# Optimization experiments

Hardware: AMD Instinct MI355X
Metric: run time of the kernel (lower is better)

## Reference

```python
import jax, jax.numpy as jnp
import numpy as np

B, N, C, T = 8, 207, 2, 12
E, HEADS, L, FF = 64, 4, 2, 4
TOUT = 12
N_GAT_HEADS = 8
ALPHA = 0.2
NEG = -9e15


def layer_norm(x, g, b, eps=1e-5):
    mu = x.mean(-1, keepdims=True)
    var = x.var(-1, keepdims=True)
    return (x - mu) / jnp.sqrt(var + eps) * g + b


def setup_inputs() -> dict:
    key = jax.random.key(0)
    ks = iter(jax.random.split(key, 40))

    def rn(shape, s=0.1):
        return jax.random.normal(next(ks), shape, jnp.float32) * s

    return {
        "x": jax.random.normal(next(ks), (B, C, N, T), jnp.float32),
        "adj": jax.random.randint(next(ks), (B, N, N), 0, 2, jnp.int32),
        # GraphAttention params per head (W1 is dead code in the original: omitted)
        "gat_W2": rn((N_GAT_HEADS, 2 * C, C), 0.5),
        "gat_a": rn((N_GAT_HEADS, C), 0.5),
        "gat_b": rn((N_GAT_HEADS, C), 0.1),
        "conv1_w": rn((2 * C, E), 0.3),   # 1x1 conv: [in, out]
        "conv1_b": rn((E,), 0.1),
        "temb": rn((288, E), 0.1),        # temporal embedding table [time_num, E]
        "Wq": rn((L, E, E), 0.12), "Wk": rn((L, E, E), 0.12), "Wv": rn((L, E, E), 0.12),
        "Wo": rn((L, E, E), 0.12), "bo": rn((L, E), 0.02),
        "ln1_g": jnp.ones((L, E)), "ln1_b": jnp.zeros((L, E)),
        "ln2_g": jnp.ones((L, E)), "ln2_b": jnp.zeros((L, E)),
        "ff_w1": rn((L, E, FF * E), 0.12), "ff_b1": rn((L, FF * E), 0.02),
        "ff_w2": rn((L, FF * E, E), 0.12), "ff_b2": rn((L, E), 0.02),
        "lng": jnp.ones((L, E)), "lnb": jnp.zeros((L, E)),
        "conv2_w": rn((TOUT, T), 0.2), "conv2_b": rn((TOUT,), 0.05),
        "conv3_w": rn((E,), 0.2), "conv3_b": rn((1,), 0.05),
    }


def reference(x, adj, gat_W2, gat_a, gat_b, conv1_w, conv1_b, temb,
              Wq, Wk, Wv, Wo, bo, ln1_g, ln1_b, ln2_g, ln2_b,
              ff_w1, ff_b1, ff_w2, ff_b2, lng, lnb,
              conv2_w, conv2_b, conv3_w, conv3_b):
    # ---- GAT applied independently per time step; fold T into batch ----
    xb = x.transpose(0, 3, 2, 1).reshape(B * T, N, C)      # [BT,N,C]
    adjb = jnp.repeat(adj, T, axis=0)                       # [BT,N,N]
    # Faithful replication of repeat_interleave / repeat + cat(dim=1) + view
    # (note: the original concatenates along dim=1 then views, which scrambles
    #  the pairwise layout; jnp reshape reproduces the identical memory view)
    comb = jnp.concatenate([jnp.repeat(xb, N, axis=1),
                            jnp.tile(xb, (1, N, 1))], axis=1).reshape(B * T, N, N, 2 * C)
    acc = jnp.zeros((B * T, N, C), x.dtype)
    for h in range(N_GAT_HEADS):  # heads have distinct params; fixed small loop
        wx = jnp.einsum('bijc,ce->bije', comb, gat_W2[h])           # [BT,N,N,C]
        e = jnp.einsum('bije,e->bij', jax.nn.leaky_relu(wx, ALPHA), gat_a[h])
        att = jax.nn.softmax(jnp.where(adjb > 0, e, NEG), axis=-1)  # [BT,N,N]
        acc = acc + jnp.tanh(jnp.einsum('bij,bjc->bic', att, xb) + gat_b[h])
    gat_out = (acc / N_GAT_HEADS).reshape(B, T, N, C)       # average aggregate

    # ---- conv1 on cat([x, GAT_feature], channel) ----
    gat_feat = gat_out.transpose(0, 3, 2, 1)                # [B,C,N,T]
    xcat = jnp.concatenate([x, gat_feat], axis=1)           # [B,2C,N,T]
    out = jnp.einsum('bcnt,ce->bnte', xcat, conv1_w) + conv1_b  # [B,N,T,E]

    # ---- temporal transformer encoder ----
    dk = E // HEADS
    scale = np.float32(1.0 / np.sqrt(dk))
    d_t = temb[:T]                                          # [T,E]
    for l in range(L):
        qq = out + d_t
        Q = (qq @ Wq[l]).reshape(B, N, T, HEADS, dk).transpose(0, 3, 1, 2, 4)
        K = (qq @ Wk[l]).reshape(B, N, T, HEADS, dk).transpose(0, 3, 1, 2, 4)
        V = (qq @ Wv[l]).reshape(B, N, T, HEADS, dk).transpose(0, 3, 1, 2, 4)
        att = jax.nn.softmax(jnp.einsum('bhntd,bhnsd->bhnts', Q, K) * scale, axis=-1)
        ctx = jnp.einsum('bhnts,bhnsd->bhntd', att, V)
        ctx = ctx.transpose(0, 2, 3, 1, 4).reshape(B, N, T, E)
        attn_out = ctx @ Wo[l] + bo[l]
        x1 = layer_norm(attn_out + qq, ln1_g[l], ln1_b[l])
        ff = jax.nn.relu(x1 @ ff_w1[l] + ff_b1[l]) @ ff_w2[l] + ff_b2[l]
        blk = layer_norm(ff + x1, ln2_g[l], ln2_b[l])
        out = layer_norm(blk + out, lng[l], lnb[l])         # outer layer norm1 residual

    # ---- output convs ----
    ot = out.transpose(0, 2, 1, 3)                          # [B,T,N,E]
    o2 = jax.nn.relu(jnp.einsum('btne,ot->bone', ot, conv2_w)
                     + conv2_b[None, :, None, None])        # [B,TOUT,N,E]
    final = jnp.einsum('btne,e->bnt', o2, conv3_w) + conv3_b[0]  # [B,N,TOUT]
    return final
```

## Files before the change

kernel.cpp:

```cpp
#include <hip/hip_runtime.h>
#include <hip/hip_bf16.h>

#define NN   207
#define BB   8
#define TT   12
#define EE   64
#define FFD  256
#define NGH  8
#define GALPHA 0.2f
#define GNEG  -9e15f

#define SRD   68
#define SRD16 72
#define FSRD  264
#define L_QQ  0
#define L_X1  816
#define L_QB  1632
#define L_KB  2064
#define L_VB  2496
#define L_SC  2928
#define L_CTX 3504
#define L_FF  1632
#define L_TOTB 4800

__device__ __forceinline__ float lo_f(unsigned u) { return __uint_as_float(u << 16); }
__device__ __forceinline__ float hi_f(unsigned u) { return __uint_as_float(u & 0xffff0000u); }
__device__ __forceinline__ float b16f(unsigned short s) { return __uint_as_float(((unsigned)s) << 16); }
__device__ __forceinline__ unsigned pk2(float a, float b) {
  unsigned la = (unsigned)__bfloat16_as_ushort(__float2bfloat16(a));
  unsigned lb = (unsigned)__bfloat16_as_ushort(__float2bfloat16(b));
  return la | (lb << 16);
}
__device__ __forceinline__ unsigned short bf16u(float a) {
  return __bfloat16_as_ushort(__float2bfloat16(a));
}
__device__ __forceinline__ float tanh_fast(float x) {
  return 1.f - 2.f * __builtin_amdgcn_rcpf(__expf(2.f * x) + 1.f);
}

__device__ __forceinline__ float row16_sum(float v) {
  v += __int_as_float(__builtin_amdgcn_update_dpp(0, __float_as_int(v), 0x121, 0xf, 0xf, false));
  v += __int_as_float(__builtin_amdgcn_update_dpp(0, __float_as_int(v), 0x122, 0xf, 0xf, false));
  v += __int_as_float(__builtin_amdgcn_update_dpp(0, __float_as_int(v), 0x124, 0xf, 0xf, false));
  v += __int_as_float(__builtin_amdgcn_update_dpp(0, __float_as_int(v), 0x128, 0xf, 0xf, false));
  return v;
}
__device__ __forceinline__ float wave_sum(float v) {
  const float r = row16_sum(v);
  const float a = __int_as_float(__builtin_amdgcn_readlane(__float_as_int(r), 0));
  const float b = __int_as_float(__builtin_amdgcn_readlane(__float_as_int(r), 16));
  const float c = __int_as_float(__builtin_amdgcn_readlane(__float_as_int(r), 32));
  const float d = __int_as_float(__builtin_amdgcn_readlane(__float_as_int(r), 48));
  return (a + b) + (c + d);
}
#define UNPK8(U, f) { (f)[0]=lo_f((U).x); (f)[1]=hi_f((U).x); (f)[2]=lo_f((U).y); (f)[3]=hi_f((U).y); \
                      (f)[4]=lo_f((U).z); (f)[5]=hi_f((U).z); (f)[6]=lo_f((U).w); (f)[7]=hi_f((U).w); }


__global__ __launch_bounds__(256) void prep_weights(
    const float* __restrict__ Wq, const float* __restrict__ Wk,
    const float* __restrict__ Wv, const float* __restrict__ Wo,
    const float* __restrict__ ff_w1, const float* __restrict__ ff_w2,
    unsigned short* __restrict__ wb)
{
  const int idx = blockIdx.x * 256 + threadIdx.x;
  float v;
  if (idx < 32768) {
    const int which = idx >> 13;
    const int r = idx & 8191;
    const int l = r >> 12, q = r & 4095;
    const int kb = q >> 9, c = (q >> 3) & 63, j = q & 7;
    const float* W = (which == 0) ? Wq : (which == 1) ? Wk : (which == 2) ? Wv : Wo;
    v = W[l*4096 + (8*kb + j)*64 + c];
  } else if (idx < 65536) {
    const int r = idx - 32768;
    const int l = r >> 14, q = r & 16383;
    const int kb = q >> 11, f = (q >> 3) & 255, j = q & 7;
    v = ff_w1[l*16384 + (8*kb + j)*256 + f];
  } else {
    const int r = idx - 65536;
    const int l = r >> 14, q = r & 16383;
    const int kb = q >> 9, e = (q >> 3) & 63, j = q & 7;
    v = ff_w2[l*16384 + (8*kb + j)*64 + e];
  }
  wb[idx] = bf16u(v);
}

#define A_GW 2484

__global__ __launch_bounds__(256) void gat_conv1_kernel(
    const float* __restrict__ x,        const int* __restrict__ adj,
    const float* __restrict__ gat_W2,   const float* __restrict__ gat_a,
    const float* __restrict__ gat_b,    const float* __restrict__ conv1_w,
    const float* __restrict__ conv1_b,  unsigned short* __restrict__ out0)
{
  __shared__ float lds[A_GW + 96];
  unsigned* au = (unsigned*)lds;

  const int bn   = blockIdx.x;
  const int b    = bn / NN;
  const int i    = bn % NN;
  const int tid  = threadIdx.x;
  const int lane = tid & 63;
  const int wid  = tid >> 6;

  const float* xb = x + b * 2 * NN * TT;
  for (int idx = tid; idx < NN * TT; idx += 256) {
    const int n = idx / TT, t = idx % TT;
    au[t * NN + n] = pk2(xb[idx], xb[NN * TT + idx]);
  }
  if (tid < 64) lds[A_GW + tid] = gat_W2[tid];
  if (tid < 16) { lds[A_GW + 64 + tid] = gat_a[tid]; lds[A_GW + 80 + tid] = gat_b[tid]; }
  __syncthreads();

  float aokf[4];
  int   row0[4], row1[4];
  {
    const int NSQ = NN * NN;
#pragma unroll
    for (int q = 0; q < 4; ++q) {
      const int j = lane + 64 * q;
      const int jj = (j < NN) ? j : 0;
      const int r0 = 2 * (i * NN + jj), r1 = r0 + 1;
      row0[q] = (r0 < NSQ) ? (r0 / NN) : ((r0 - NSQ) % NN);
      row1[q] = (r1 < NSQ) ? (r1 / NN) : ((r1 - NSQ) % NN);
      aokf[q] = ((j < NN) && adj[(b * NN + i) * NN + jj] > 0) ? 1.f : 0.f;
    }
  }

  float xr00[3][4], xr01[3][4], xr10[3][4], xr11[3][4], xj0[3][4], xj1[3][4];
#pragma unroll
  for (int tk = 0; tk < 3; ++tk) {
    const unsigned* xst = au + (wid + 4 * tk) * NN;
#pragma unroll
    for (int q = 0; q < 4; ++q) {
      int j = lane + 64 * q; if (j >= NN) j = 0;
      const unsigned u0 = xst[row0[q]], u1 = xst[row1[q]], uj = xst[j];
      xr00[tk][q] = lo_f(u0); xr01[tk][q] = hi_f(u0);
      xr10[tk][q] = lo_f(u1); xr11[tk][q] = hi_f(u1);
      xj0[tk][q]  = lo_f(uj); xj1[tk][q]  = hi_f(uj);
    }
  }

  float acc0[3] = {0.f, 0.f, 0.f}, acc1[3] = {0.f, 0.f, 0.f};
#pragma unroll 1
  for (int h = 0; h < NGH; ++h) {
    const float w0 = lds[A_GW + h*8 + 0], w1_ = lds[A_GW + h*8 + 1];
    const float w2_= lds[A_GW + h*8 + 2], w3  = lds[A_GW + h*8 + 3];
    const float w4 = lds[A_GW + h*8 + 4], w5  = lds[A_GW + h*8 + 5];
    const float w6 = lds[A_GW + h*8 + 6], w7  = lds[A_GW + h*8 + 7];
    const float a0 = lds[A_GW + 64 + h*2], a1 = lds[A_GW + 64 + h*2 + 1];
    const float gb0 = lds[A_GW + 80 + h*2], gb1 = lds[A_GW + 80 + h*2 + 1];
    float s0[3] = {0.f,0.f,0.f}, s1[3] = {0.f,0.f,0.f}, s2[3] = {0.f,0.f,0.f};
#pragma unroll
    for (int tk = 0; tk < 3; ++tk) {
#pragma unroll
      for (int q = 0; q < 4; ++q) {
        float wx0 = xr00[tk][q]*w0 + xr01[tk][q]*w2_ + xr10[tk][q]*w4 + xr11[tk][q]*w6;
        float wx1 = xr00[tk][q]*w1_ + xr01[tk][q]*w3 + xr10[tk][q]*w5 + xr11[tk][q]*w7;
        wx0 = (wx0 > 0.f) ? wx0 : GALPHA * wx0;
        wx1 = (wx1 > 0.f) ? wx1 : GALPHA * wx1;
        float e = a0 * wx0 + a1 * wx1;
        e = (aokf[q] > 0.f) ? e : GNEG;
        const float ex = __expf(e);
        s0[tk] += ex; s1[tk] += ex * xj0[tk][q]; s2[tk] += ex * xj1[tk][q];
      }
    }
#pragma unroll
    for (int tk = 0; tk < 3; ++tk) {
      const float d0 = wave_sum(s0[tk]);
      const float d1 = wave_sum(s1[tk]);
      const float d2 = wave_sum(s2[tk]);
      const float inv = __builtin_amdgcn_rcpf(d0);
      acc0[tk] += tanh_fast(d1 * inv + gb0);
      acc1[tk] += tanh_fast(d2 * inv + gb1);
    }
  }

  {
    const float c1w0 = conv1_w[lane],       c1w1 = conv1_w[64 + lane];
    const float c1w2 = conv1_w[128 + lane], c1w3 = conv1_w[192 + lane];
    const float c1b  = conv1_b[lane];
#pragma unroll
    for (int tk = 0; tk < 3; ++tk) {
      const int t = wid + 4 * tk;
      const unsigned up = au[t * NN + i];
      const float g0 = acc0[tk] * (1.f / NGH), g1 = acc1[tk] * (1.f / NGH);
      out0[bn*768 + t*EE + lane] =
          bf16u(lo_f(up)*c1w0 + hi_f(up)*c1w1 + g0*c1w2 + g1*c1w3 + c1b);
    }
  }
}

__global__ __launch_bounds__(256) void xf_final_kernel(
    const unsigned short* __restrict__ out0,
    const unsigned short* __restrict__ wb,
    const float* __restrict__ temb,
    const float* __restrict__ bo,
    const float* __restrict__ ln1_g, const float* __restrict__ ln1_b,
    const float* __restrict__ ln2_g, const float* __restrict__ ln2_b,
    const float* __restrict__ ff_b1, const float* __restrict__ ff_b2,
    const float* __restrict__ lng, const float* __restrict__ lnb,
    const float* __restrict__ conv2_w, const float* __restrict__ conv2_b,
    const float* __restrict__ conv3_w, const float* __restrict__ conv3_b,
    float* __restrict__ fout)
{
  __shared__ float lds[L_TOTB];
  unsigned*       au   = (unsigned*)lds;
  unsigned short* sh16 = (unsigned short*)lds;

  const int bn   = blockIdx.x;
  const int tid  = threadIdx.x;
  const int lane = tid & 63;
  const int wid  = tid >> 6;
  const int t0   = 3 * wid;

  float outv[3];
#pragma unroll
  for (int tt = 0; tt < 3; ++tt)
    outv[tt] = b16f(out0[bn*768 + (t0 + tt)*EE + lane]);

  for (int l = 0; l < 2; ++l) {
    const unsigned short* wqt = wb + l*4096;
    const unsigned short* wkt = wb + 8192  + l*4096;
    const unsigned short* wvt = wb + 16384 + l*4096;
    const unsigned short* wot = wb + 24576 + l*4096;
    const unsigned short* w1t = wb + 32768 + l*16384;
    const unsigned short* w2t = wb + 65536 + l*16384;

    __syncthreads();

    float qqv[3];
#pragma unroll
    for (int tt = 0; tt < 3; ++tt) {
      qqv[tt] = outv[tt] + temb[(t0 + tt)*EE + lane];
      lds[L_QQ + (t0 + tt)*SRD + lane] = qqv[tt];
    }

    {
      const int c = lane;
      float aq[3] = {0,0,0}, ak[3] = {0,0,0}, av[3] = {0,0,0};
      const unsigned short* wqp = wqt + c*8;
      const unsigned short* wkp = wkt + c*8;
      const unsigned short* wvp = wvt + c*8;
#pragma unroll 1
      for (int kb = 0; kb < 8; ++kb) {
        const uint4 wq4 = *(const uint4*)(wqp + kb*512);
        const uint4 wk4 = *(const uint4*)(wkp + kb*512);
        const uint4 wv4 = *(const uint4*)(wvp + kb*512);
        float a[3][8];
#pragma unroll
        for (int tt = 0; tt < 3; ++tt) {
          *(float4*)&a[tt][0] = *(const float4*)&lds[L_QQ + (t0+tt)*SRD + 8*kb];
          *(float4*)&a[tt][4] = *(const float4*)&lds[L_QQ + (t0+tt)*SRD + 8*kb + 4];
        }
        float wf[8];
        UNPK8(wq4, wf);
#pragma unroll
        for (int tt = 0; tt < 3; ++tt)
#pragma unroll
          for (int j = 0; j < 8; ++j) aq[tt] += a[tt][j]*wf[j];
        UNPK8(wk4, wf);
#pragma unroll
        for (int tt = 0; tt < 3; ++tt)
#pragma unroll
          for (int j = 0; j < 8; ++j) ak[tt] += a[tt][j]*wf[j];
        UNPK8(wv4, wf);
#pragma unroll
        for (int tt = 0; tt < 3; ++tt)
#pragma unroll
          for (int j = 0; j < 8; ++j) av[tt] += a[tt][j]*wf[j];
      }
#pragma unroll
      for (int tt = 0; tt < 3; ++tt) {
        const int t = t0 + tt;
        sh16[2*L_QB + t*SRD16 + c] = bf16u(aq[tt]);
        sh16[2*L_KB + t*SRD16 + c] = bf16u(ak[tt]);
        sh16[2*L_VB + t*SRD16 + c] = bf16u(av[tt]);
      }
    }
    __syncthreads();

    {
      const int h = wid;
      if (lane < 48) {
        const int t = lane >> 2, s0 = 3*(lane & 3);
        float qf[16];
        {
          const uint4 qa = *(const uint4*)&sh16[2*L_QB + t*SRD16 + h*16];
          const uint4 qb = *(const uint4*)&sh16[2*L_QB + t*SRD16 + h*16 + 8];
          UNPK8(qa, qf); UNPK8(qb, qf + 8);
        }
#pragma unroll
        for (int ss = 0; ss < 3; ++ss) {
          const int s = s0 + ss;
          float d = 0.f;
          {
            const uint4 ka = *(const uint4*)&sh16[2*L_KB + s*SRD16 + h*16];
            float kf[8]; UNPK8(ka, kf);
#pragma unroll
            for (int xq = 0; xq < 8; ++xq) d += qf[xq]*kf[xq];
          }
          {
            const uint4 kc = *(const uint4*)&sh16[2*L_KB + s*SRD16 + h*16 + 8];
            float kf[8]; UNPK8(kc, kf);
#pragma unroll
            for (int xq = 0; xq < 8; ++xq) d += qf[8+xq]*kf[xq];
          }
          lds[L_SC + h*144 + t*12 + s] = d * 0.25f;
        }
      }
      __builtin_amdgcn_wave_barrier();
      if (lane < 12) {
        float* row = &lds[L_SC + h*144 + lane*12];
        float m = row[0];
#pragma unroll
        for (int s = 1; s < 12; ++s) m = fmaxf(m, row[s]);
        float ex[12]; float sum = 0.f;
#pragma unroll
        for (int s = 0; s < 12; ++s) { ex[s] = __expf(row[s] - m); sum += ex[s]; }
        const float inv = __builtin_amdgcn_rcpf(sum);
#pragma unroll
        for (int s = 0; s < 12; ++s) row[s] = ex[s] * inv;
      }
      __builtin_amdgcn_wave_barrier();
      {
        const int d = lane & 15, tq = lane >> 4;
#pragma unroll
        for (int tt = 0; tt < 3; ++tt) {
          const int t = tq + 4*tt;
          float cacc = 0.f;
#pragma unroll
          for (int s = 0; s < 12; ++s) {
            const float p = lds[L_SC + h*144 + t*12 + s];
            const unsigned uv = au[L_VB + s*36 + h*8 + (d >> 1)];
            cacc += p * ((d & 1) ? hi_f(uv) : lo_f(uv));
          }
          lds[L_CTX + t*SRD + h*16 + d] = cacc;
        }
      }
    }
    __syncthreads();

    {
      float acc[3] = {0,0,0};
      const unsigned short* wop = wot + lane*8;
#pragma unroll 1
      for (int kb = 0; kb < 8; ++kb) {
        const uint4 w4 = *(const uint4*)(wop + kb*512);
        float a[3][8];
#pragma unroll
        for (int tt = 0; tt < 3; ++tt) {
          *(float4*)&a[tt][0] = *(const float4*)&lds[L_CTX + (t0+tt)*SRD + 8*kb];
          *(float4*)&a[tt][4] = *(const float4*)&lds[L_CTX + (t0+tt)*SRD + 8*kb + 4];
        }
        float wf[8]; UNPK8(w4, wf);
#pragma unroll
        for (int tt = 0; tt < 3; ++tt)
#pragma unroll
          for (int j = 0; j < 8; ++j) acc[tt] += a[tt][j]*wf[j];
      }
#pragma unroll
      for (int tt = 0; tt < 3; ++tt) {
        float v = acc[tt] + bo[l*EE + lane] + qqv[tt];
        const float mu = wave_sum(v) * (1.f/64);
        const float dd = v - mu;
        const float var = wave_sum(dd*dd) * (1.f/64);
        lds[L_X1 + (t0+tt)*SRD + lane] =
            dd * rsqrtf(var + 1e-5f) * ln1_g[l*EE + lane] + ln1_b[l*EE + lane];
      }
    }
    __syncthreads();

    {
      const int f0 = 4*lane;
      float ac[4][3] = {};
#pragma unroll 1
      for (int kb = 0; kb < 8; ++kb) {
        uint4 w4[4];
#pragma unroll
        for (int ff = 0; ff < 4; ++ff)
          w4[ff] = *(const uint4*)(w1t + kb*2048 + (f0+ff)*8);
        float a[3][8];
#pragma unroll
        for (int tt = 0; tt < 3; ++tt) {
          *(float4*)&a[tt][0] = *(const float4*)&lds[L_X1 + (t0+tt)*SRD + 8*kb];
          *(float4*)&a[tt][4] = *(const float4*)&lds[L_X1 + (t0+tt)*SRD + 8*kb + 4];
        }
#pragma unroll
        for (int ff = 0; ff < 4; ++ff) {
          float wf[8]; UNPK8(w4[ff], wf);
#pragma unroll
          for (int tt = 0; tt < 3; ++tt)
#pragma unroll
            for (int j = 0; j < 8; ++j) ac[ff][tt] += a[tt][j]*wf[j];
        }
      }
      const float4 bv = *(const float4*)&ff_b1[l*FFD + f0];
#pragma unroll
      for (int tt = 0; tt < 3; ++tt) {
        *(float4*)&lds[L_FF + (t0+tt)*FSRD + f0] = make_float4(
            fmaxf(ac[0][tt] + bv.x, 0.f), fmaxf(ac[1][tt] + bv.y, 0.f),
            fmaxf(ac[2][tt] + bv.z, 0.f), fmaxf(ac[3][tt] + bv.w, 0.f));
      }
    }

    {
      float acc[3] = {0,0,0};
      const unsigned short* w2p = w2t + lane*8;
#pragma unroll 1
      for (int kb = 0; kb < 32; ++kb) {
        const uint4 w4 = *(const uint4*)(w2p + kb*512);
        float a[3][8];
#pragma unroll
        for (int tt = 0; tt < 3; ++tt) {
          *(float4*)&a[tt][0] = *(const float4*)&lds[L_FF + (t0+tt)*FSRD + 8*kb];
          *(float4*)&a[tt][4] = *(const float4*)&lds[L_FF + (t0+tt)*FSRD + 8*kb + 4];
        }
        float wf[8]; UNPK8(w4, wf);
#pragma unroll
        for (int tt = 0; tt < 3; ++tt)
#pragma unroll
          for (int j = 0; j < 8; ++j) acc[tt] += a[tt][j]*wf[j];
      }
#pragma unroll
      for (int tt = 0; tt < 3; ++tt) {
        float v = acc[tt] + ff_b2[l*EE + lane] + lds[L_X1 + (t0+tt)*SRD + lane];
        float mu = wave_sum(v) * (1.f/64);
        float dd = v - mu;
        float var = wave_sum(dd*dd) * (1.f/64);
        const float blk = dd * rsqrtf(var + 1e-5f) * ln2_g[l*EE + lane] + ln2_b[l*EE + lane];
        float w = blk + outv[tt];
        mu = wave_sum(w) * (1.f/64);
        dd = w - mu;
        var = wave_sum(dd*dd) * (1.f/64);
        outv[tt] = dd * rsqrtf(var + 1e-5f) * lng[l*EE + lane] + lnb[l*EE + lane];
      }
    }
  }

#pragma unroll
  for (int tt = 0; tt < 3; ++tt)
    lds[L_QQ + (t0+tt)*SRD + lane] = outv[tt];
  __syncthreads();

  float xt[12];
#pragma unroll
  for (int t = 0; t < 12; ++t) xt[t] = lds[L_QQ + t*SRD + lane];
  const float c3w = conv3_w[lane];
  for (int o = wid; o < 12; o += 4) {
    float a = conv2_b[o];
#pragma unroll
    for (int t = 0; t < 12; ++t) a += xt[t] * conv2_w[o*TT + t];
    a = fmaxf(a, 0.f);
    const float s = wave_sum(a * c3w);
    if (lane == 0) fout[bn*TT + o] = s + conv3_b[0];
  }
}

extern "C" void kernel_launch(void* const* d_in, const int* in_sizes, int n_in,
                              void* d_out, int out_size, void* d_ws, size_t ws_size,
                              hipStream_t stream) {
  const float* x       = (const float*)d_in[0];
  const int*   adj     = (const int*)  d_in[1];
  const float* gat_W2  = (const float*)d_in[2];
  const float* gat_a   = (const float*)d_in[3];
  const float* gat_b   = (const float*)d_in[4];
  const float* conv1_w = (const float*)d_in[5];
  const float* conv1_b = (const float*)d_in[6];
  const float* temb    = (const float*)d_in[7];
  const float* Wq      = (const float*)d_in[8];
  const float* Wk      = (const float*)d_in[9];
  const float* Wv      = (const float*)d_in[10];
  const float* Wo      = (const float*)d_in[11];
  const float* bo      = (const float*)d_in[12];
  const float* ln1_g   = (const float*)d_in[13];
  const float* ln1_b   = (const float*)d_in[14];
  const float* ln2_g   = (const float*)d_in[15];
  const float* ln2_b   = (const float*)d_in[16];
  const float* ff_w1   = (const float*)d_in[17];
  const float* ff_b1   = (const float*)d_in[18];
  const float* ff_w2   = (const float*)d_in[19];
  const float* ff_b2   = (const float*)d_in[20];
  const float* lng     = (const float*)d_in[21];
  const float* lnb     = (const float*)d_in[22];
  const float* conv2_w = (const float*)d_in[23];
  const float* conv2_b = (const float*)d_in[24];
  const float* conv3_w = (const float*)d_in[25];
  const float* conv3_b = (const float*)d_in[26];

  unsigned short* wb   = (unsigned short*)d_ws;
  unsigned short* out0 = wb + 98304;
  float* fout = (float*)d_out;

  prep_weights<<<384, 256, 0, stream>>>(Wq, Wk, Wv, Wo, ff_w1, ff_w2, wb);

  gat_conv1_kernel<<<BB*NN, 256, 0, stream>>>(
      x, adj, gat_W2, gat_a, gat_b, conv1_w, conv1_b, out0);

  xf_final_kernel<<<BB*NN, 256, 0, stream>>>(
      out0, wb, temb, bo, ln1_g, ln1_b, ln2_g, ln2_b,
      ff_b1, ff_b2, lng, lnb, conv2_w, conv2_b, conv3_w, conv3_b, fout);
}
```

Baseline: 283.9 us.

## Switch transformer matmuls to packed fp16 FMA with fp16 activations in LDS

Stores weights, the intermediate activation buffer and the LDS activations as fp16 instead of bf16/fp32, and runs the QKV, score, output projection and FFN dot products with packed half2 FMAs (v_pk_fma_f16) in place of unpacked fp32 FMAs. The LDS layout is redone with disjoint regions per tensor so some __syncthreads can be dropped, and the post-attention LN1 result is kept in registers. This roughly halves FMA instruction count and LDS traffic. The cost is fp16 accumulation, with a risk of lost precision or overflow over the 256-long FFN reductions.

```diff
diff --git a/kernel.cpp b/kernel.cpp
--- a/kernel.cpp
+++ b/kernel.cpp
@@ -1,5 +1,6 @@
 #include <hip/hip_runtime.h>
 #include <hip/hip_bf16.h>
+#include <hip/hip_fp16.h>
 
 #define NN   207
 #define BB   8
@@ -10,29 +11,29 @@
 #define GALPHA 0.2f
 #define GNEG  -9e15f
 
-#define SRD   68
-#define SRD16 72
-#define FSRD  264
-#define L_QQ  0
-#define L_X1  816
-#define L_QB  1632
-#define L_KB  2064
-#define L_VB  2496
-#define L_SC  2928
-#define L_CTX 3504
-#define L_FF  1632
-#define L_TOTB 4800
+#define U_QQ  0
+#define U_X1  864
+#define U_QB  1728
+#define U_KB  2592
+#define U_VB  3456
+#define F_SC  2160
+#define U_CTX 5472
+#define U_FF  6336
+#define F_FIN 3168
+#define LDS_F32 4752
 
 __device__ __forceinline__ float lo_f(unsigned u) { return __uint_as_float(u << 16); }
 __device__ __forceinline__ float hi_f(unsigned u) { return __uint_as_float(u & 0xffff0000u); }
-__device__ __forceinline__ float b16f(unsigned short s) { return __uint_as_float(((unsigned)s) << 16); }
 __device__ __forceinline__ unsigned pk2(float a, float b) {
   unsigned la = (unsigned)__bfloat16_as_ushort(__float2bfloat16(a));
   unsigned lb = (unsigned)__bfloat16_as_ushort(__float2bfloat16(b));
   return la | (lb << 16);
 }
-__device__ __forceinline__ unsigned short bf16u(float a) {
-  return __bfloat16_as_ushort(__float2bfloat16(a));
+__device__ __forceinline__ unsigned short h16u(float a) {
+  return __half_as_ushort(__float2half(a));
+}
+__device__ __forceinline__ float u16f(unsigned short s) {
+  return __half2float(__ushort_as_half(s));
 }
 __device__ __forceinline__ float tanh_fast(float x) {
   return 1.f - 2.f * __builtin_amdgcn_rcpf(__expf(2.f * x) + 1.f);
@@ -53,8 +54,6 @@
   const float d = __int_as_float(__builtin_amdgcn_readlane(__float_as_int(r), 48));
   return (a + b) + (c + d);
 }
-#define UNPK8(U, f) { (f)[0]=lo_f((U).x); (f)[1]=hi_f((U).x); (f)[2]=lo_f((U).y); (f)[3]=hi_f((U).y); \
-                      (f)[4]=lo_f((U).z); (f)[5]=hi_f((U).z); (f)[6]=lo_f((U).w); (f)[7]=hi_f((U).w); }
 
 
 __global__ __launch_bounds__(256) void prep_weights(
@@ -83,7 +82,7 @@
     const int kb = q >> 9, e = (q >> 3) & 63, j = q & 7;
     v = ff_w2[l*16384 + (8*kb + j)*64 + e];
   }
-  wb[idx] = bf16u(v);
+  wb[idx] = h16u(v);
 }
 
 #define A_GW 2484
@@ -187,7 +186,7 @@
       const unsigned up = au[t * NN + i];
       const float g0 = acc0[tk] * (1.f / NGH), g1 = acc1[tk] * (1.f / NGH);
       out0[bn*768 + t*EE + lane] =
-          bf16u(lo_f(up)*c1w0 + hi_f(up)*c1w1 + g0*c1w2 + g1*c1w3 + c1b);
+          h16u(lo_f(up)*c1w0 + hi_f(up)*c1w1 + g0*c1w2 + g1*c1w3 + c1b);
     }
   }
 }
@@ -205,7 +204,7 @@
     const float* __restrict__ conv3_w, const float* __restrict__ conv3_b,
     float* __restrict__ fout)
 {
-  __shared__ float lds[L_TOTB];
+  __shared__ float lds[LDS_F32];
   unsigned*       au   = (unsigned*)lds;
   unsigned short* sh16 = (unsigned short*)lds;
 
@@ -215,10 +214,12 @@
   const int wid  = tid >> 6;
   const int t0   = 3 * wid;
 
+  const __half2 hz = __floats2half2_rn(0.f, 0.f);
+
   float outv[3];
 #pragma unroll
   for (int tt = 0; tt < 3; ++tt)
-    outv[tt] = b16f(out0[bn*768 + (t0 + tt)*EE + lane]);
+    outv[tt] = u16f(out0[bn*768 + (t0 + tt)*EE + lane]);
 
   for (int l = 0; l < 2; ++l) {
     const unsigned short* wqt = wb + l*4096;
@@ -228,55 +229,49 @@
     const unsigned short* w1t = wb + 32768 + l*16384;
     const unsigned short* w2t = wb + 65536 + l*16384;
 
-    __syncthreads();
-
     float qqv[3];
 #pragma unroll
     for (int tt = 0; tt < 3; ++tt) {
       qqv[tt] = outv[tt] + temb[(t0 + tt)*EE + lane];
-      lds[L_QQ + (t0 + tt)*SRD + lane] = qqv[tt];
+      sh16[U_QQ + (t0 + tt)*72 + lane] = h16u(qqv[tt]);
     }
 
     {
-      const int c = lane;
-      float aq[3] = {0,0,0}, ak[3] = {0,0,0}, av[3] = {0,0,0};
-      const unsigned short* wqp = wqt + c*8;
-      const unsigned short* wkp = wkt + c*8;
-      const unsigned short* wvp = wvt + c*8;
+      const unsigned short* wqp = wqt + lane*8;
+      const unsigned short* wkp = wkt + lane*8;
+      const unsigned short* wvp = wvt + lane*8;
+      __half2 cq[3], ck[3], cv[3];
+#pragma unroll
+      for (int tt = 0; tt < 3; ++tt) { cq[tt] = hz; ck[tt] = hz; cv[tt] = hz; }
 #pragma unroll 1
       for (int kb = 0; kb < 8; ++kb) {
         const uint4 wq4 = *(const uint4*)(wqp + kb*512);
         const uint4 wk4 = *(const uint4*)(wkp + kb*512);
         const uint4 wv4 = *(const uint4*)(wvp + kb*512);
-        float a[3][8];
+        uint4 a4[3];
+#pragma unroll
+        for (int tt = 0; tt < 3; ++tt)
+          a4[tt] = *(const uint4*)&sh16[U_QQ + (t0+tt)*72 + 8*kb];
+        const __half2* wq2 = (const __half2*)&wq4;
+        const __half2* wk2 = (const __half2*)&wk4;
+        const __half2* wv2 = (const __half2*)&wv4;
 #pragma unroll
         for (int tt = 0; tt < 3; ++tt) {
-          *(float4*)&a[tt][0] = *(const float4*)&lds[L_QQ + (t0+tt)*SRD + 8*kb];
-          *(float4*)&a[tt][4] = *(const float4*)&lds[L_QQ + (t0+tt)*SRD + 8*kb + 4];
-        }
-        float wf[8];
-        UNPK8(wq4, wf);
-#pragma unroll
-        for (int tt = 0; tt < 3; ++tt)
-#pragma unroll
-          for (int j = 0; j < 8; ++j) aq[tt] += a[tt][j]*wf[j];
-        UNPK8(wk4, wf);
-#pragma unroll
-        for (int tt = 0; tt < 3; ++tt)
-#pragma unroll
-          for (int j = 0; j < 8; ++j) ak[tt] += a[tt][j]*wf[j];
-        UNPK8(wv4, wf);
-#pragma unroll
-        for (int tt = 0; tt < 3; ++tt)
-#pragma unroll
-          for (int j = 0; j < 8; ++j) av[tt] += a[tt][j]*wf[j];
+          const __half2* a2 = (const __half2*)&a4[tt];
+#pragma unroll
+          for (int j = 0; j < 4; ++j) {
+            cq[tt] = __hfma2(a2[j], wq2[j], cq[tt]);
+            ck[tt] = __hfma2(a2[j], wk2[j], ck[tt]);
+            cv[tt] = __hfma2(a2[j], wv2[j], cv[tt]);
+          }
+        }
       }
 #pragma unroll
       for (int tt = 0; tt < 3; ++tt) {
         const int t = t0 + tt;
-        sh16[2*L_QB + t*SRD16 + c] = bf16u(aq[tt]);
-        sh16[2*L_KB + t*SRD16 + c] = bf16u(ak[tt]);
-        sh16[2*L_VB + t*SRD16 + c] = bf16u(av[tt]);
+        sh16[U_QB + t*72 + lane] = h16u(__low2float(cq[tt]) + __high2float(cq[tt]));
+        sh16[U_KB + t*72 + lane] = h16u(__low2float(ck[tt]) + __high2float(ck[tt]));
+        sh16[U_VB + t*72 + lane] = h16u(__low2float(cv[tt]) + __high2float(cv[tt]));
       }
     }
     __syncthreads();
@@ -285,34 +280,29 @@
       const int h = wid;
       if (lane < 48) {
         const int t = lane >> 2, s0 = 3*(lane & 3);
-        float qf[16];
-        {
-          const uint4 qa = *(const uint4*)&sh16[2*L_QB + t*SRD16 + h*16];
-          const uint4 qb = *(const uint4*)&sh16[2*L_QB + t*SRD16 + h*16 + 8];
-          UNPK8(qa, qf); UNPK8(qb, qf + 8);
-        }
+        const uint4 qa = *(const uint4*)&sh16[U_QB + t*72 + h*16];
+        const uint4 qb = *(const uint4*)&sh16[U_QB + t*72 + h*16 + 8];
+        const __half2* q2a = (const __half2*)&qa;
+        const __half2* q2b = (const __half2*)&qb;
 #pragma unroll
         for (int ss = 0; ss < 3; ++ss) {
           const int s = s0 + ss;
-          float d = 0.f;
-          {
-            const uint4 ka = *(const uint4*)&sh16[2*L_KB + s*SRD16 + h*16];
-            float kf[8]; UNPK8(ka, kf);
-#pragma unroll
-            for (int xq = 0; xq < 8; ++xq) d += qf[xq]*kf[xq];
+          const uint4 ka = *(const uint4*)&sh16[U_KB + s*72 + h*16];
+          const uint4 kc = *(const uint4*)&sh16[U_KB + s*72 + h*16 + 8];
+          const __half2* k2a = (const __half2*)&ka;
+          const __half2* k2b = (const __half2*)&kc;
+          __half2 d2 = hz;
+#pragma unroll
+          for (int j = 0; j < 4; ++j) {
+            d2 = __hfma2(q2a[j], k2a[j], d2);
+            d2 = __hfma2(q2b[j], k2b[j], d2);
           }
-          {
-            const uint4 kc = *(const uint4*)&sh16[2*L_KB + s*SRD16 + h*16 + 8];
-            float kf[8]; UNPK8(kc, kf);
-#pragma unroll
-            for (int xq = 0; xq < 8; ++xq) d += qf[8+xq]*kf[xq];
-          }
-          lds[L_SC + h*144 + t*12 + s] = d * 0.25f;
+          lds[F_SC + h*144 + t*12 + s] = (__low2float(d2) + __high2float(d2)) * 0.25f;
         }
       }
       __builtin_amdgcn_wave_barrier();
       if (lane < 12) {
-        float* row = &lds[L_SC + h*144 + lane*12];
+        float* row = &lds[F_SC + h*144 + lane*12];
         float m = row[0];
 #pragma unroll
         for (int s = 1; s < 12; ++s) m = fmaxf(m, row[s]);
@@ -332,100 +322,130 @@
           float cacc = 0.f;
 #pragma unroll
           for (int s = 0; s < 12; ++s) {
-            const float p = lds[L_SC + h*144 + t*12 + s];
-            const unsigned uv = au[L_VB + s*36 + h*8 + (d >> 1)];
-            cacc += p * ((d & 1) ? hi_f(uv) : lo_f(uv));
+            const float p = lds[F_SC + h*144 + t*12 + s];
+            const unsigned uv = au[(U_VB/2) + s*36 + h*8 + (d >> 1)];
+            const __half2 hv = *(const __half2*)&uv;
+            cacc += p * ((d & 1) ? __high2float(hv) : __low2float(hv));
           }
-          lds[L_CTX + t*SRD + h*16 + d] = cacc;
+          sh16[U_CTX + t*72 + h*16 + d] = h16u(cacc);
         }
       }
     }
     __syncthreads();
 
+    float x1v[3];
     {
-      float acc[3] = {0,0,0};
       const unsigned short* wop = wot + lane*8;
+      __half2 co[3];
+#pragma unroll
+      for (int tt = 0; tt < 3; ++tt) co[tt] = hz;
 #pragma unroll 1
       for (int kb = 0; kb < 8; ++kb) {
         const uint4 w4 = *(const uint4*)(wop + kb*512);
-        float a[3][8];
+        const __half2* w2_ = (const __half2*)&w4;
+        uint4 a4[3];
+#pragma unroll
+        for (int tt = 0; tt < 3; ++tt)
+          a4[tt] = *(const uint4*)&sh16[U_CTX + (t0+tt)*72 + 8*kb];
 #pragma unroll
         for (int tt = 0; tt < 3; ++tt) {
-          *(float4*)&a[tt][0] = *(const float4*)&lds[L_CTX + (t0+tt)*SRD + 8*kb];
-          *(float4*)&a[tt][4] = *(const float4*)&lds[L_CTX + (t0+tt)*SRD + 8*kb + 4];
-        }
-        float wf[8]; UNPK8(w4, wf);
-#pragma unroll
-        for (int tt = 0; tt < 3; ++tt)
-#pragma unroll
-          for (int j = 0; j < 8; ++j) acc[tt] += a[tt][j]*wf[j];
+          const __half2* a2 = (const __half2*)&a4[tt];
+#pragma unroll
+          for (int j = 0; j < 4; ++j) co[tt] = __hfma2(a2[j], w2_[j], co[tt]);
+        }
       }
 #pragma unroll
       for (int tt = 0; tt < 3; ++tt) {
-        float v = acc[tt] + bo[l*EE + lane] + qqv[tt];
+        float v = __low2float(co[tt]) + __high2float(co[tt]) + bo[l*EE + lane] + qqv[tt];
         const float mu = wave_sum(v) * (1.f/64);
         const float dd = v - mu;
         const float var = wave_sum(dd*dd) * (1.f/64);
-        lds[L_X1 + (t0+tt)*SRD + lane] =
-            dd * rsqrtf(var + 1e-5f) * ln1_g[l*EE + lane] + ln1_b[l*EE + lane];
-      }
-    }
-    __syncthreads();
+        x1v[tt] = dd * rsqrtf(var + 1e-5f) * ln1_g[l*EE + lane] + ln1_b[l*EE + lane];
+        sh16[U_X1 + (t0+tt)*72 + lane] = h16u(x1v[tt]);
+      }
+    }
 
     {
       const int f0 = 4*lane;
-      float ac[4][3] = {};
+      __half2 c2[4][3];
+#pragma unroll
+      for (int ff = 0; ff < 4; ++ff)
+#pragma unroll
+        for (int tt = 0; tt < 3; ++tt) c2[ff][tt] = hz;
 #pragma unroll 1
       for (int kb = 0; kb < 8; ++kb) {
         uint4 w4[4];
 #pragma unroll
         for (int ff = 0; ff < 4; ++ff)
           w4[ff] = *(const uint4*)(w1t + kb*2048 + (f0+ff)*8);
-        float a[3][8];
-#pragma unroll
-        for (int tt = 0; tt < 3; ++tt) {
-          *(float4*)&a[tt][0] = *(const float4*)&lds[L_X1 + (t0+tt)*SRD + 8*kb];
-          *(float4*)&a[tt][4] = *(const float4*)&lds[L_X1 + (t0+tt)*SRD + 8*kb + 4];
-        }
+        uint4 a4[3];
+#pragma unroll
+        for (int tt = 0; tt < 3; ++tt)
+          a4[tt] = *(const uint4*)&sh16[U_X1 + (t0+tt)*72 + 8*kb];
 #pragma unroll
         for (int ff = 0; ff < 4; ++ff) {
-          float wf[8]; UNPK8(w4[ff], wf);
-#pragma unroll
-          for (int tt = 0; tt < 3; ++tt)
-#pragma unroll
-            for (int j = 0; j < 8; ++j) ac[ff][tt] += a[tt][j]*wf[j];
+          const __half2* w2_ = (const __half2*)&w4[ff];
+#pragma unroll
+          for (int tt = 0; tt < 3; ++tt) {
+            const __half2* a2 = (const __half2*)&a4[tt];
+#pragma unroll
+            for (int j = 0; j < 4; ++j) c2[ff][tt] = __hfma2(a2[j], w2_[j], c2[ff][tt]);
+          }
         }
       }
       const float4 bv = *(const float4*)&ff_b1[l*FFD + f0];
 #pragma unroll
       for (int tt = 0; tt < 3; ++tt) {
-        *(float4*)&lds[L_FF + (t0+tt)*FSRD + f0] = make_float4(
-            fmaxf(ac[0][tt] + bv.x, 0.f), fmaxf(ac[1][tt] + bv.y, 0.f),
-            fmaxf(ac[2][tt] + bv.z, 0.f), fmaxf(ac[3][tt] + bv.w, 0.f));
+        const float r0 = fmaxf(__low2float(c2[0][tt]) + __high2float(c2[0][tt]) + bv.x, 0.f);
+        const float r1 = fmaxf(__low2float(c2[1][tt]) + __high2float(c2[1][tt]) + bv.y, 0.f);
+        const float r2 = fmaxf(__low2float(c2[2][tt]) + __high2float(c2[2][tt]) + bv.z, 0.f);
+        const float r3 = fmaxf(__low2float(c2[3][tt]) + __high2float(c2[3][tt]) + bv.w, 0.f);
+        __half2 p01 = __floats2half2_rn(r0, r1);
+        __half2 p23 = __floats2half2_rn(r2, r3);
+        uint2 pk;
+        pk.x = *(unsigned*)&p01;
+        pk.y = *(unsigned*)&p23;
+        *(uint2*)&sh16[U_FF + (t0+tt)*264 + f0] = pk;
       }
     }
 
     {
-      float acc[3] = {0,0,0};
       const unsigned short* w2p = w2t + lane*8;
+      __half2 cA[3], cB[3];
+#pragma unroll
+      for (int tt = 0; tt < 3; ++tt) { cA[tt] = hz; cB[tt] = hz; }
 #pragma unroll 1
-      for (int kb = 0; kb < 32; ++kb) {
-        const uint4 w4 = *(const uint4*)(w2p + kb*512);
-        float a[3][8];
-#pragma unroll
-        for (int tt = 0; tt < 3; ++tt) {
-          *(float4*)&a[tt][0] = *(const float4*)&lds[L_FF + (t0+tt)*FSRD + 8*kb];
-          *(float4*)&a[tt][4] = *(const float4*)&lds[L_FF + (t0+tt)*FSRD + 8*kb + 4];
-        }
-        float wf[8]; UNPK8(w4, wf);
-#pragma unroll
-        for (int tt = 0; tt < 3; ++tt)
-#pragma unroll
-          for (int j = 0; j < 8; ++j) acc[tt] += a[tt][j]*wf[j];
+      for (int kp = 0; kp < 16; ++kp) {
+        {
+          const int kb = 2*kp;
+          const uint4 w4 = *(const uint4*)(w2p + kb*512);
+          const __half2* w2_ = (const __half2*)&w4;
+#pragma unroll
+          for (int tt = 0; tt < 3; ++tt) {
+            const uint4 a4 = *(const uint4*)&sh16[U_FF + (t0+tt)*264 + 8*kb];
+            const __half2* a2 = (const __half2*)&a4;
+#pragma unroll
+            for (int j = 0; j < 4; ++j) cA[tt] = __hfma2(a2[j], w2_[j], cA[tt]);
+          }
+        }
+        {
+          const int kb = 2*kp + 1;
+          const uint4 w4 = *(const uint4*)(w2p + kb*512);
+          const __half2* w2_ = (const __half2*)&w4;
+#pragma unroll
+          for (int tt = 0; tt < 3; ++tt) {
+            const uint4 a4 = *(const uint4*)&sh16[U_FF + (t0+tt)*264 + 8*kb];
+            const __half2* a2 = (const __half2*)&a4;
+#pragma unroll
+            for (int j = 0; j < 4; ++j) cB[tt] = __hfma2(a2[j], w2_[j], cB[tt]);
+          }
+        }
       }
 #pragma unroll
       for (int tt = 0; tt < 3; ++tt) {
-        float v = acc[tt] + ff_b2[l*EE + lane] + lds[L_X1 + (t0+tt)*SRD + lane];
+        float v = __low2float(cA[tt]) + __high2float(cA[tt])
+                + __low2float(cB[tt]) + __high2float(cB[tt])
+                + ff_b2[l*EE + lane] + x1v[tt];
         float mu = wave_sum(v) * (1.f/64);
         float dd = v - mu;
         float var = wave_sum(dd*dd) * (1.f/64);
@@ -439,14 +459,15 @@
     }
   }
 
+  __syncthreads();
 #pragma unroll
   for (int tt = 0; tt < 3; ++tt)
-    lds[L_QQ + (t0+tt)*SRD + lane] = outv[tt];
+    lds[F_FIN + (t0+tt)*68 + lane] = outv[tt];
   __syncthreads();
 
   float xt[12];
 #pragma unroll
-  for (int t = 0; t < 12; ++t) xt[t] = lds[L_QQ + t*SRD + lane];
+  for (int t = 0; t < 12; ++t) xt[t] = lds[F_FIN + t*68 + lane];
   const float c3w = conv3_w[lane];
   for (int o = wid; o < 12; o += 4) {
     float a = conv2_b[o];
```

Result: faster. 236.0 us (-16.9%).
